# Kernel optimization log

Hardware: AMD Instinct MI355X
Metric: run time of the kernel (lower is better)

The kernel has to match this reference:

```python
import jax, jax.numpy as jnp
import numpy as np

B, N, D, P, H, DH = 1, 1536, 512, 64, 16, 64
INNER = H * DH  # 1024

def _ln(x, g, b, eps=1e-5):
    m = jnp.mean(x, axis=-1, keepdims=True)
    v = jnp.var(x, axis=-1, keepdims=True)
    return (x - m) / jnp.sqrt(v + eps) * g + b

def setup_inputs() -> dict:
    key = jax.random.key(0)
    ks = jax.random.split(key, 10)
    s = 0.02
    return {
        "node_feats": jax.random.normal(ks[0], (B, N, D), jnp.float32),
        "pair_feats": jax.random.normal(ks[1], (B, N, N, P), jnp.float32),
        "mask": jnp.ones((B, N, N), dtype=bool),
        "ln_node_g": jnp.ones((D,), jnp.float32), "ln_node_b": jnp.zeros((D,), jnp.float32),
        "ln_pair_g": jnp.ones((P,), jnp.float32), "ln_pair_b": jnp.zeros((P,), jnp.float32),
        "Wq": s * jax.random.normal(ks[2], (D, INNER), jnp.float32),
        "bq": jnp.zeros((INNER,), jnp.float32),
        "Wkv": s * jax.random.normal(ks[3], (D, 2 * INNER), jnp.float32),
        "bkv": jnp.zeros((2 * INNER,), jnp.float32),
        "qln_g": jnp.ones((INNER,), jnp.float32), "qln_b": jnp.zeros((INNER,), jnp.float32),
        "kln_g": jnp.ones((INNER,), jnp.float32), "kln_b": jnp.zeros((INNER,), jnp.float32),
        "Wg": s * jax.random.normal(ks[4], (D, INNER), jnp.float32),
        "bg": jnp.zeros((INNER,), jnp.float32),
        "Wbias": s * jax.random.normal(ks[5], (P, H), jnp.float32),
        "Wout": s * jax.random.normal(ks[6], (INNER, D), jnp.float32),
        "bout": jnp.zeros((D,), jnp.float32),
        "n_queries": 0,
        "n_keys": 0,
    }

def reference(node_feats, pair_feats, mask, ln_node_g, ln_node_b, ln_pair_g, ln_pair_b,
              Wq, bq, Wkv, bkv, qln_g, qln_b, kln_g, kln_b, Wg, bg, Wbias, Wout, bout,
              n_queries, n_keys):
    b, n, _ = node_feats.shape
    x = _ln(node_feats, ln_node_g, ln_node_b)          # [b,n,D]
    p = _ln(pair_feats, ln_pair_g, ln_pair_b)          # [b,n,n,P]
    q = _ln(x @ Wq + bq, qln_g, qln_b)                 # [b,n,I]
    kv = x @ Wkv + bkv
    k, v = jnp.split(kv, 2, axis=-1)
    k = _ln(k, kln_g, kln_b)
    g = x @ Wg + bg                                    # gating, [b,n,I]
    bias = jnp.einsum('bijp,ph->bhij', p, Wbias)       # pair bias, [b,h,n,n]
    # split heads -> [b,h,n,dh]
    split = lambda t: t.reshape(b, n, H, DH).transpose(0, 2, 1, 3)
    qh, kh, vh, gh = split(q), split(k), split(v), split(g)
    scale = DH ** -0.5
    sim = jnp.einsum('bhid,bhjd->bhij', qh, kh) * scale
    sim = jnp.where(mask[:, None, :, :], sim, jnp.finfo(sim.dtype).min)
    attn = jax.nn.softmax(sim + bias, axis=-1)
    o = jnp.einsum('bhij,bhjd->bhid', attn, vh)        # [b,h,n,dh]
    o = jax.nn.sigmoid(gh) * o
    o = o.transpose(0, 2, 1, 3).reshape(b, n, INNER)
    return o @ Wout + bout
```

## Files before the change

kernel.cpp:

```cpp
#include <hip/hip_runtime.h>

#define NN 1536
#define DD 512
#define PP 64
#define HH 16
#define DHD 64
#define INNER 1024
#define NCHUNK 4
#define JT_PER (NN / 64 / NCHUNK)

typedef __attribute__((ext_vector_type(4))) float f32x4;
typedef __attribute__((ext_vector_type(8))) _Float16 f16x8;
typedef __attribute__((ext_vector_type(4))) _Float16 f16x4;

__device__ inline float wave_sum(float v) {
#pragma unroll
  for (int m = 1; m <= 32; m <<= 1) v += __shfl_xor(v, m);
  return v;
}

__global__ __launch_bounds__(256) void transpose_f32_f16(const float* __restrict__ in,
    _Float16* __restrict__ out, int R, int C) {
  __shared__ float tile[64][65];
  int c0 = blockIdx.x * 64, r0 = blockIdx.y * 64;
  int tid = threadIdx.x;
  int ri = tid >> 4, ci = (tid & 15) * 4;
#pragma unroll
  for (int p = 0; p < 4; ++p) {
    float4 v = *(const float4*)&in[(size_t)(r0 + ri + p * 16) * C + c0 + ci];
    tile[ri + p * 16][ci + 0] = v.x;
    tile[ri + p * 16][ci + 1] = v.y;
    tile[ri + p * 16][ci + 2] = v.z;
    tile[ri + p * 16][ci + 3] = v.w;
  }
  __syncthreads();
  int wr = tid >> 3, wc = (tid & 7) * 8;
#pragma unroll
  for (int p = 0; p < 2; ++p) {
    f16x8 o;
#pragma unroll
    for (int jj = 0; jj < 8; ++jj) o[jj] = (_Float16)tile[wc + jj][wr + p * 32];
    *(f16x8*)&out[(size_t)(c0 + wr + p * 32) * R + r0 + wc] = o;
  }
}

__global__ __launch_bounds__(256) void transpose_qkvg(const float* __restrict__ Wq,
    const float* __restrict__ Wkv, const float* __restrict__ Wg,
    _Float16* __restrict__ BTall) {
  int cg0 = blockIdx.x * 64;
  const float* src; int Cs, c0;
  if (cg0 < 1024)      { src = Wq;  Cs = 1024; c0 = cg0; }
  else if (cg0 < 3072) { src = Wkv; Cs = 2048; c0 = cg0 - 1024; }
  else                 { src = Wg;  Cs = 1024; c0 = cg0 - 3072; }
  __shared__ float tile[64][65];
  int r0 = blockIdx.y * 64;
  int tid = threadIdx.x;
  int ri = tid >> 4, ci = (tid & 15) * 4;
#pragma unroll
  for (int p = 0; p < 4; ++p) {
    float4 v = *(const float4*)&src[(size_t)(r0 + ri + p * 16) * Cs + c0 + ci];
    tile[ri + p * 16][ci + 0] = v.x;
    tile[ri + p * 16][ci + 1] = v.y;
    tile[ri + p * 16][ci + 2] = v.z;
    tile[ri + p * 16][ci + 3] = v.w;
  }
  __syncthreads();
  int wr = tid >> 3, wc = (tid & 7) * 8;
#pragma unroll
  for (int p = 0; p < 2; ++p) {
    f16x8 o;
#pragma unroll
    for (int jj = 0; jj < 8; ++jj) o[jj] = (_Float16)tile[wc + jj][wr + p * 32];
    *(f16x8*)&BTall[(size_t)(cg0 + wr + p * 32) * DD + r0 + wc] = o;
  }
}

__global__ __launch_bounds__(256) void transpose_f16_b(const _Float16* __restrict__ in0,
    _Float16* __restrict__ out0, int R, int C) {
  const _Float16* in = in0 + (size_t)blockIdx.z * R * C;
  _Float16* out = out0 + (size_t)blockIdx.z * R * C;
  __shared__ _Float16 tile[64][72];
  int c0 = blockIdx.x * 64, r0 = blockIdx.y * 64;
  int tid = threadIdx.x;
  int ri = tid >> 3, ci = (tid & 7) * 8;
#pragma unroll
  for (int p = 0; p < 2; ++p)
    *(f16x8*)&tile[ri + p * 32][ci] = *(const f16x8*)&in[(size_t)(r0 + ri + p * 32) * C + c0 + ci];
  __syncthreads();
#pragma unroll
  for (int p = 0; p < 2; ++p) {
    f16x8 o;
#pragma unroll
    for (int jj = 0; jj < 8; ++jj) o[jj] = tile[ci + jj][ri + p * 32];
    *(f16x8*)&out[(size_t)(c0 + ri + p * 32) * R + r0 + ci] = o;
  }
}

__global__ __launch_bounds__(256) void node_ln_kernel(const float* __restrict__ nf,
    const float* __restrict__ g, const float* __restrict__ b, _Float16* __restrict__ x16) {
  int i = blockIdx.x, tid = threadIdx.x;
  int c = tid * 2;
  float2 v = *(const float2*)&nf[(size_t)i * DD + c];
  float s = v.x + v.y, ss = v.x * v.x + v.y * v.y;
  s = wave_sum(s); ss = wave_sum(ss);
  __shared__ float red[2][4];
  int w = tid >> 6;
  if ((tid & 63) == 0) { red[0][w] = s; red[1][w] = ss; }
  __syncthreads();
  s = red[0][0] + red[0][1] + red[0][2] + red[0][3];
  ss = red[1][0] + red[1][1] + red[1][2] + red[1][3];
  float mean = s * (1.f / DD);
  float var = ss * (1.f / DD) - mean * mean;
  float rstd = rsqrtf(var + 1e-5f);
  x16[(size_t)i * DD + c + 0] = (_Float16)((v.x - mean) * rstd * g[c + 0] + b[c + 0]);
  x16[(size_t)i * DD + c + 1] = (_Float16)((v.y - mean) * rstd * g[c + 1] + b[c + 1]);
}

__global__ __launch_bounds__(256) void gemm_proj(const _Float16* __restrict__ A,
    const _Float16* __restrict__ BT, const float* __restrict__ bq,
    const float* __restrict__ bkv, const float* __restrict__ bg,
    float* __restrict__ C) {
  __shared__ _Float16 As[64][72];
  __shared__ _Float16 Bs[64][72];
  int tid = threadIdx.x, lane = tid & 63, w = tid >> 6;
  int m0 = blockIdx.y * 64, n0 = blockIdx.x * 64;
  int wm = (w & 1) * 32, wn = (w >> 1) * 32;
  f32x4 acc[2][2] = {};
  int r = tid >> 3, c8 = (tid & 7) * 8;
  int lr = lane & 15, lg = lane >> 4;
  for (int k0 = 0; k0 < DD; k0 += 64) {
    *(f16x8*)&As[r][c8]      = *(const f16x8*)&A[(size_t)(m0 + r) * DD + k0 + c8];
    *(f16x8*)&As[r + 32][c8] = *(const f16x8*)&A[(size_t)(m0 + r + 32) * DD + k0 + c8];
    *(f16x8*)&Bs[r][c8]      = *(const f16x8*)&BT[(size_t)(n0 + r) * DD + k0 + c8];
    *(f16x8*)&Bs[r + 32][c8] = *(const f16x8*)&BT[(size_t)(n0 + r + 32) * DD + k0 + c8];
    __syncthreads();
#pragma unroll
    for (int kf = 0; kf < 2; ++kf) {
      f16x8 a0 = *(const f16x8*)&As[wm + lr][kf * 32 + lg * 8];
      f16x8 a1 = *(const f16x8*)&As[wm + 16 + lr][kf * 32 + lg * 8];
      f16x8 b0 = *(const f16x8*)&Bs[wn + lr][kf * 32 + lg * 8];
      f16x8 b1 = *(const f16x8*)&Bs[wn + 16 + lr][kf * 32 + lg * 8];
      acc[0][0] = __builtin_amdgcn_mfma_f32_16x16x32_f16(a0, b0, acc[0][0], 0, 0, 0);
      acc[0][1] = __builtin_amdgcn_mfma_f32_16x16x32_f16(a0, b1, acc[0][1], 0, 0, 0);
      acc[1][0] = __builtin_amdgcn_mfma_f32_16x16x32_f16(a1, b0, acc[1][0], 0, 0, 0);
      acc[1][1] = __builtin_amdgcn_mfma_f32_16x16x32_f16(a1, b1, acc[1][1], 0, 0, 0);
    }
    __syncthreads();
  }
#pragma unroll
  for (int mi = 0; mi < 2; ++mi)
#pragma unroll
    for (int ni = 0; ni < 2; ++ni)
#pragma unroll
      for (int rg = 0; rg < 4; ++rg) {
        int row = m0 + wm + mi * 16 + lg * 4 + rg;
        int col = n0 + wn + ni * 16 + lr;
        float bv = (col < 1024) ? bq[col] : (col < 3072) ? bkv[col - 1024] : bg[col - 3072];
        C[(size_t)row * 4096 + col] = acc[mi][ni][rg] + bv;
      }
}

__global__ __launch_bounds__(256) void gemm_f16(const _Float16* __restrict__ A,
    const _Float16* __restrict__ BT, const float* __restrict__ bias,
    float* __restrict__ C, int M, int N, int K) {
  __shared__ _Float16 As[64][72];
  __shared__ _Float16 Bs[64][72];
  int tid = threadIdx.x, lane = tid & 63, w = tid >> 6;
  int m0 = blockIdx.y * 64, n0 = blockIdx.x * 64;
  int wm = (w & 1) * 32, wn = (w >> 1) * 32;
  f32x4 acc[2][2] = {};
  int r = tid >> 3, c8 = (tid & 7) * 8;
  int lr = lane & 15, lg = lane >> 4;
  for (int k0 = 0; k0 < K; k0 += 64) {
    *(f16x8*)&As[r][c8]      = *(const f16x8*)&A[(size_t)(m0 + r) * K + k0 + c8];
    *(f16x8*)&As[r + 32][c8] = *(const f16x8*)&A[(size_t)(m0 + r + 32) * K + k0 + c8];
    *(f16x8*)&Bs[r][c8]      = *(const f16x8*)&BT[(size_t)(n0 + r) * K + k0 + c8];
    *(f16x8*)&Bs[r + 32][c8] = *(const f16x8*)&BT[(size_t)(n0 + r + 32) * K + k0 + c8];
    __syncthreads();
#pragma unroll
    for (int kf = 0; kf < 2; ++kf) {
      f16x8 a0 = *(const f16x8*)&As[wm + lr][kf * 32 + lg * 8];
      f16x8 a1 = *(const f16x8*)&As[wm + 16 + lr][kf * 32 + lg * 8];
      f16x8 b0 = *(const f16x8*)&Bs[wn + lr][kf * 32 + lg * 8];
      f16x8 b1 = *(const f16x8*)&Bs[wn + 16 + lr][kf * 32 + lg * 8];
      acc[0][0] = __builtin_amdgcn_mfma_f32_16x16x32_f16(a0, b0, acc[0][0], 0, 0, 0);
      acc[0][1] = __builtin_amdgcn_mfma_f32_16x16x32_f16(a0, b1, acc[0][1], 0, 0, 0);
      acc[1][0] = __builtin_amdgcn_mfma_f32_16x16x32_f16(a1, b0, acc[1][0], 0, 0, 0);
      acc[1][1] = __builtin_amdgcn_mfma_f32_16x16x32_f16(a1, b1, acc[1][1], 0, 0, 0);
    }
    __syncthreads();
  }
#pragma unroll
  for (int mi = 0; mi < 2; ++mi)
#pragma unroll
    for (int ni = 0; ni < 2; ++ni)
#pragma unroll
      for (int rg = 0; rg < 4; ++rg) {
        int row = m0 + wm + mi * 16 + lg * 4 + rg;
        int col = n0 + wn + ni * 16 + lr;
        C[(size_t)row * N + col] = acc[mi][ni][rg] + bias[col];
      }
}

__global__ __launch_bounds__(256) void qkv_ln_kernel(const float* __restrict__ prebuf,
    const float* __restrict__ qg, const float* __restrict__ qb,
    const float* __restrict__ kg, const float* __restrict__ kb,
    _Float16* __restrict__ q16, _Float16* __restrict__ k16, _Float16* __restrict__ v16) {
  int i = blockIdx.x, tid = threadIdx.x;
  int c = tid * 4;
  const float* rowp = &prebuf[(size_t)i * 4096];
  float4 qv = *(const float4*)&rowp[c];
  float4 kvv = *(const float4*)&rowp[1024 + c];
  float4 vv = *(const float4*)&rowp[2048 + c];
  float qs = qv.x + qv.y + qv.z + qv.w;
  float qss = qv.x * qv.x + qv.y * qv.y + qv.z * qv.z + qv.w * qv.w;
  float ks = kvv.x + kvv.y + kvv.z + kvv.w;
  float kss = kvv.x * kvv.x + kvv.y * kvv.y + kvv.z * kvv.z + kvv.w * kvv.w;
  qs = wave_sum(qs); qss = wave_sum(qss); ks = wave_sum(ks); kss = wave_sum(kss);
  __shared__ float red[4][4];
  int w = tid >> 6;
  if ((tid & 63) == 0) { red[0][w] = qs; red[1][w] = qss; red[2][w] = ks; red[3][w] = kss; }
  __syncthreads();
  qs = red[0][0] + red[0][1] + red[0][2] + red[0][3];
  qss = red[1][0] + red[1][1] + red[1][2] + red[1][3];
  ks = red[2][0] + red[2][1] + red[2][2] + red[2][3];
  kss = red[3][0] + red[3][1] + red[3][2] + red[3][3];
  float qm = qs * (1.f / INNER), qvr = qss * (1.f / INNER) - qm * qm, qr = rsqrtf(qvr + 1e-5f);
  float km = ks * (1.f / INNER), kvr = kss * (1.f / INNER) - km * km, kr = rsqrtf(kvr + 1e-5f);
  int hh = c >> 6, d = c & 63;
  size_t off = ((size_t)hh * NN + i) * DHD + d;
  f16x4 qo, ko, vo;
  qo[0] = (_Float16)((qv.x - qm) * qr * qg[c + 0] + qb[c + 0]);
  qo[1] = (_Float16)((qv.y - qm) * qr * qg[c + 1] + qb[c + 1]);
  qo[2] = (_Float16)((qv.z - qm) * qr * qg[c + 2] + qb[c + 2]);
  qo[3] = (_Float16)((qv.w - qm) * qr * qg[c + 3] + qb[c + 3]);
  ko[0] = (_Float16)((kvv.x - km) * kr * kg[c + 0] + kb[c + 0]);
  ko[1] = (_Float16)((kvv.y - km) * kr * kg[c + 1] + kb[c + 1]);
  ko[2] = (_Float16)((kvv.z - km) * kr * kg[c + 2] + kb[c + 2]);
  ko[3] = (_Float16)((kvv.w - km) * kr * kg[c + 3] + kb[c + 3]);
  vo[0] = (_Float16)vv.x; vo[1] = (_Float16)vv.y; vo[2] = (_Float16)vv.z; vo[3] = (_Float16)vv.w;
  *(f16x4*)&q16[off] = qo;
  *(f16x4*)&k16[off] = ko;
  *(f16x4*)&v16[off] = vo;
}

__global__ __launch_bounds__(256) void pair_bias_kernel(const float* __restrict__ pair,
    const float* __restrict__ pg, const float* __restrict__ pb,
    const float* __restrict__ Wbias, _Float16* __restrict__ bias16) {
  int i = blockIdx.x;
  int tid = threadIdx.x, lane = tid & 63, w = tid >> 6;
  int lj = lane & 15, pbase = (lane >> 4) * 8;
  f16x8 wb0, wb1;
#pragma unroll
  for (int jj = 0; jj < 8; ++jj) {
    wb0[jj] = (_Float16)Wbias[(pbase + jj) * HH + lj];
    wb1[jj] = (_Float16)Wbias[(pbase + 32 + jj) * HH + lj];
  }
  float4 g0 = *(const float4*)&pg[pbase],      g1 = *(const float4*)&pg[pbase + 4];
  float4 g2 = *(const float4*)&pg[pbase + 32], g3 = *(const float4*)&pg[pbase + 36];
  float4 b0 = *(const float4*)&pb[pbase],      b1 = *(const float4*)&pb[pbase + 4];
  float4 b2 = *(const float4*)&pb[pbase + 32], b3 = *(const float4*)&pb[pbase + 36];
  __shared__ _Float16 trans[16][72];
  for (int t4 = 0; t4 < 4; ++t4) {
    int jt0 = blockIdx.y * 256 + t4 * 64;
    int j = jt0 + w * 16 + lj;
    const float* src = &pair[((size_t)i * NN + j) * PP];
    float4 v0 = *(const float4*)&src[pbase];
    float4 v1 = *(const float4*)&src[pbase + 4];
    float4 v2 = *(const float4*)&src[pbase + 32];
    float4 v3 = *(const float4*)&src[pbase + 36];
    float s = v0.x + v0.y + v0.z + v0.w + v1.x + v1.y + v1.z + v1.w
            + v2.x + v2.y + v2.z + v2.w + v3.x + v3.y + v3.z + v3.w;
    float ss = v0.x * v0.x + v0.y * v0.y + v0.z * v0.z + v0.w * v0.w
             + v1.x * v1.x + v1.y * v1.y + v1.z * v1.z + v1.w * v1.w
             + v2.x * v2.x + v2.y * v2.y + v2.z * v2.z + v2.w * v2.w
             + v3.x * v3.x + v3.y * v3.y + v3.z * v3.z + v3.w * v3.w;
    s += __shfl_xor(s, 16); s += __shfl_xor(s, 32);
    ss += __shfl_xor(ss, 16); ss += __shfl_xor(ss, 32);
    float mean = s * (1.f / PP);
    float var = ss * (1.f / PP) - mean * mean;
    float rstd = rsqrtf(var + 1e-5f);
    f16x8 a0, a1;
    a0[0] = (_Float16)((v0.x - mean) * rstd * g0.x + b0.x);
    a0[1] = (_Float16)((v0.y - mean) * rstd * g0.y + b0.y);
    a0[2] = (_Float16)((v0.z - mean) * rstd * g0.z + b0.z);
    a0[3] = (_Float16)((v0.w - mean) * rstd * g0.w + b0.w);
    a0[4] = (_Float16)((v1.x - mean) * rstd * g1.x + b1.x);
    a0[5] = (_Float16)((v1.y - mean) * rstd * g1.y + b1.y);
    a0[6] = (_Float16)((v1.z - mean) * rstd * g1.z + b1.z);
    a0[7] = (_Float16)((v1.w - mean) * rstd * g1.w + b1.w);
    a1[0] = (_Float16)((v2.x - mean) * rstd * g2.x + b2.x);
    a1[1] = (_Float16)((v2.y - mean) * rstd * g2.y + b2.y);
    a1[2] = (_Float16)((v2.z - mean) * rstd * g2.z + b2.z);
    a1[3] = (_Float16)((v2.w - mean) * rstd * g2.w + b2.w);
    a1[4] = (_Float16)((v3.x - mean) * rstd * g3.x + b3.x);
    a1[5] = (_Float16)((v3.y - mean) * rstd * g3.y + b3.y);
    a1[6] = (_Float16)((v3.z - mean) * rstd * g3.z + b3.z);
    a1[7] = (_Float16)((v3.w - mean) * rstd * g3.w + b3.w);
    f32x4 cacc = {};
    cacc = __builtin_amdgcn_mfma_f32_16x16x32_f16(a0, wb0, cacc, 0, 0, 0);
    cacc = __builtin_amdgcn_mfma_f32_16x16x32_f16(a1, wb1, cacc, 0, 0, 0);
#pragma unroll
    for (int rg = 0; rg < 4; ++rg)
      trans[lj][w * 16 + (lane >> 4) * 4 + rg] = (_Float16)cacc[rg];
    __syncthreads();
    int hh = tid >> 4, jc = (tid & 15) * 4;
    f16x4 ov = *(const f16x4*)&trans[hh][jc];
    *(f16x4*)&bias16[((size_t)hh * NN + i) * NN + jt0 + jc] = ov;
    __syncthreads();
  }
}

__global__ __launch_bounds__(256) void attn_kernel(const _Float16* __restrict__ q16,
    const _Float16* __restrict__ k16, const _Float16* __restrict__ vT16,
    const _Float16* __restrict__ bias16, float* __restrict__ opart,
    float* __restrict__ mlbuf) {
  int it = blockIdx.x, h = blockIdx.y, ck = blockIdx.z;
  int tid = threadIdx.x, lane = tid & 63, w = tid >> 6;
  int lr = lane & 15, lg = lane >> 4;
  __shared__ _Float16 Kt[64][72];
  __shared__ _Float16 Vt[64][72];
  __shared__ _Float16 Bls[64][72];
  int ib0 = it * 64;
  int ib = ib0 + w * 16;
  f16x8 qb0 = *(const f16x8*)&q16[((size_t)h * NN + ib + lr) * DHD + lg * 8];
  f16x8 qb1 = *(const f16x8*)&q16[((size_t)h * NN + ib + lr) * DHD + 32 + lg * 8];
  float m = -INFINITY, lsum = 0.f;
  f32x4 oacc[4] = {};
  int sr = tid >> 3, sc = (tid & 7) * 8;
  for (int jt = ck * JT_PER; jt < (ck + 1) * JT_PER; ++jt) {
    int j0 = jt * 64;
    *(f16x8*)&Kt[sr][sc]      = *(const f16x8*)&k16[((size_t)h * NN + j0 + sr) * DHD + sc];
    *(f16x8*)&Kt[sr + 32][sc] = *(const f16x8*)&k16[((size_t)h * NN + j0 + sr + 32) * DHD + sc];
    *(f16x8*)&Vt[sr][sc]      = *(const f16x8*)&vT16[((size_t)h * DHD + sr) * NN + j0 + sc];
    *(f16x8*)&Vt[sr + 32][sc] = *(const f16x8*)&vT16[((size_t)h * DHD + sr + 32) * NN + j0 + sc];
    *(f16x8*)&Bls[sr][sc]      = *(const f16x8*)&bias16[((size_t)h * NN + ib0 + sr) * NN + j0 + sc];
    *(f16x8*)&Bls[sr + 32][sc] = *(const f16x8*)&bias16[((size_t)h * NN + ib0 + sr + 32) * NN + j0 + sc];
    __syncthreads();
    float s[4][4];
#pragma unroll
    for (int jq = 0; jq < 4; ++jq) {
      f16x8 ka0 = *(const f16x8*)&Kt[jq * 16 + lr][lg * 8];
      f16x8 ka1 = *(const f16x8*)&Kt[jq * 16 + lr][32 + lg * 8];
      f32x4 c = {};
      c = __builtin_amdgcn_mfma_f32_16x16x32_f16(ka0, qb0, c, 0, 0, 0);
      c = __builtin_amdgcn_mfma_f32_16x16x32_f16(ka1, qb1, c, 0, 0, 0);
      f16x4 bls = *(const f16x4*)&Bls[w * 16 + lr][jq * 16 + lg * 4];
#pragma unroll
      for (int r = 0; r < 4; ++r)
        s[jq][r] = c[r] * 0.125f + (float)bls[r];
    }
    float tmax = s[0][0];
#pragma unroll
    for (int jq = 0; jq < 4; ++jq)
#pragma unroll
      for (int r = 0; r < 4; ++r) tmax = fmaxf(tmax, s[jq][r]);
    tmax = fmaxf(tmax, __shfl_xor(tmax, 16));
    tmax = fmaxf(tmax, __shfl_xor(tmax, 32));
    float mn = fmaxf(m, tmax);
    float alpha = __expf(m - mn);
    float ps = 0.f;
    f16x4 pf[4];
#pragma unroll
    for (int jq = 0; jq < 4; ++jq)
#pragma unroll
      for (int r = 0; r < 4; ++r) {
        float p = __expf(s[jq][r] - mn);
        ps += p;
        pf[jq][r] = (_Float16)p;
      }
    ps += __shfl_xor(ps, 16);
    ps += __shfl_xor(ps, 32);
    lsum = lsum * alpha + ps;
    m = mn;
    float ar[4];
#pragma unroll
    for (int r = 0; r < 4; ++r) ar[r] = __shfl(alpha, lg * 4 + r);
#pragma unroll
    for (int dt = 0; dt < 4; ++dt)
#pragma unroll
      for (int r = 0; r < 4; ++r) oacc[dt][r] *= ar[r];
#pragma unroll
    for (int dt = 0; dt < 4; ++dt)
#pragma unroll
      for (int jq = 0; jq < 4; ++jq) {
        f16x4 vb = *(const f16x4*)&Vt[dt * 16 + lr][jq * 16 + lg * 4];
        oacc[dt] = __builtin_amdgcn_mfma_f32_16x16x16f16(pf[jq], vb, oacc[dt], 0, 0, 0);
      }
    __syncthreads();
  }
  size_t pbase = (((size_t)it * HH + h) * NCHUNK + ck) * 4096 + (size_t)w * 1024;
#pragma unroll
  for (int dt = 0; dt < 4; ++dt)
    *(f32x4*)&opart[pbase + dt * 256 + lane * 4] = oacc[dt];
  if (lg == 0) {
    size_t mb = (((size_t)it * HH + h) * NCHUNK + ck) * 128;
    mlbuf[mb + w * 16 + lr] = m;
    mlbuf[mb + 64 + w * 16 + lr] = lsum;
  }
}

__global__ __launch_bounds__(256) void attn_merge(const float* __restrict__ opart,
    const float* __restrict__ mlbuf, const float* __restrict__ prebuf,
    _Float16* __restrict__ o16) {
  int it = blockIdx.x, h = blockIdx.y;
  int tid = threadIdx.x, lane = tid & 63, w = tid >> 6;
  int lr = lane & 15, lg = lane >> 4;
  __shared__ float sm[NCHUNK][64], sl[NCHUNK][64];
  {
    int c = tid >> 6, i = tid & 63;
    size_t mb = (((size_t)it * HH + h) * NCHUNK + c) * 128;
    sm[c][i] = mlbuf[mb + i];
    sl[c][i] = mlbuf[mb + 64 + i];
  }
  __syncthreads();
  float wc[NCHUNK][4], linv[4];
#pragma unroll
  for (int r = 0; r < 4; ++r) {
    int i_loc = w * 16 + lg * 4 + r;
    float mg = sm[0][i_loc];
#pragma unroll
    for (int c = 1; c < NCHUNK; ++c) mg = fmaxf(mg, sm[c][i_loc]);
    float lt = 0.f;
#pragma unroll
    for (int c = 0; c < NCHUNK; ++c) {
      float e = __expf(sm[c][i_loc] - mg);
      wc[c][r] = e;
      lt += e * sl[c][i_loc];
    }
    linv[r] = 1.f / lt;
  }
  size_t base = ((size_t)it * HH + h) * NCHUNK * 4096 + (size_t)w * 1024;
#pragma unroll
  for (int dt = 0; dt < 4; ++dt) {
    f32x4 o = {};
#pragma unroll
    for (int c = 0; c < NCHUNK; ++c) {
      f32x4 v = *(const f32x4*)&opart[base + (size_t)c * 4096 + dt * 256 + lane * 4];
#pragma unroll
      for (int r = 0; r < 4; ++r) o[r] += wc[c][r] * v[r];
    }
    int d = dt * 16 + lr;
#pragma unroll
    for (int r = 0; r < 4; ++r) {
      int i = it * 64 + w * 16 + lg * 4 + r;
      float gt = prebuf[(size_t)i * 4096 + 3072 + h * DHD + d];
      float val = o[r] * linv[r] * (1.f / (1.f + __expf(-gt)));
      o16[(size_t)i * INNER + h * DHD + d] = (_Float16)val;
    }
  }
}

extern "C" void kernel_launch(void* const* d_in, const int* in_sizes, int n_in,
                              void* d_out, int out_size, void* d_ws, size_t ws_size,
                              hipStream_t stream) {
  const float* node  = (const float*)d_in[0];
  const float* pair  = (const float*)d_in[1];
  const float* ln_ng = (const float*)d_in[3];
  const float* ln_nb = (const float*)d_in[4];
  const float* ln_pg = (const float*)d_in[5];
  const float* ln_pb = (const float*)d_in[6];
  const float* Wq    = (const float*)d_in[7];
  const float* bq    = (const float*)d_in[8];
  const float* Wkv   = (const float*)d_in[9];
  const float* bkv   = (const float*)d_in[10];
  const float* qlg   = (const float*)d_in[11];
  const float* qlb   = (const float*)d_in[12];
  const float* klg   = (const float*)d_in[13];
  const float* klb   = (const float*)d_in[14];
  const float* Wg    = (const float*)d_in[15];
  const float* bg    = (const float*)d_in[16];
  const float* Wbias = (const float*)d_in[17];
  const float* Wout  = (const float*)d_in[18];
  const float* bout  = (const float*)d_in[19];
  float* out = (float*)d_out;

  char* ws = (char*)d_ws;
  const size_t MB = 1u << 20;
  _Float16* BTall  = (_Float16*)(ws + 0 * MB);
  _Float16* WoutT  = (_Float16*)(ws + 4 * MB);
  _Float16* x16    = (_Float16*)(ws + 5 * MB);
  float*    prebuf = (float*)(ws + 8 * MB);
  _Float16* q16    = (_Float16*)(ws + 32 * MB);
  _Float16* k16    = (_Float16*)(ws + 35 * MB);
  _Float16* v16    = (_Float16*)(ws + 38 * MB);
  _Float16* vT16   = (_Float16*)(ws + 41 * MB);
  _Float16* o16    = (_Float16*)(ws + 44 * MB);
  _Float16* bias16 = (_Float16*)(ws + 48 * MB);
  float*    opart  = (float*)(ws + 124 * MB);
  float*    mlbuf  = (float*)(ws + 150 * MB);

  transpose_qkvg<<<dim3(4096 / 64, DD / 64), 256, 0, stream>>>(Wq, Wkv, Wg, BTall);
  transpose_f32_f16<<<dim3(DD / 64, INNER / 64), 256, 0, stream>>>(Wout, WoutT, INNER, DD);

  node_ln_kernel<<<NN, 256, 0, stream>>>(node, ln_ng, ln_nb, x16);

  gemm_proj<<<dim3(4096 / 64, NN / 64), 256, 0, stream>>>(x16, BTall, bq, bkv, bg, prebuf);

  qkv_ln_kernel<<<NN, 256, 0, stream>>>(prebuf, qlg, qlb, klg, klb, q16, k16, v16);

  transpose_f16_b<<<dim3(1, NN / 64, HH), 256, 0, stream>>>(v16, vT16, NN, DHD);

  pair_bias_kernel<<<dim3(NN, NN / 256), 256, 0, stream>>>(pair, ln_pg, ln_pb, Wbias, bias16);

  attn_kernel<<<dim3(NN / 64, HH, NCHUNK), 256, 0, stream>>>(q16, k16, vT16, bias16, opart, mlbuf);

  attn_merge<<<dim3(NN / 64, HH), 256, 0, stream>>>(opart, mlbuf, prebuf, o16);

  gemm_f16<<<dim3(DD / 64, NN / 64), 256, 0, stream>>>(o16, WoutT, bout, out, NN, DD, INNER);
}
```

Measured before the change: 278.8 us.

## Fuse pair-bias LayerNorm projection into attention and store intermediates in fp16

Pair LayerNorm and the bias projection now run inside the attention kernel. Each block handles 16 query rows by 192 keys for all 16 heads and keeps the bias tile in LDS, so the 75MB fp16 bias tensor is never written to or read back from global memory. The projection buffer and the partial outputs are now stored in fp16, and the key range is split into 8 chunks instead of 4. K and V are read straight from global or L2 instead of being staged in LDS, and the larger register footprint may lower occupancy.

```diff
diff --git a/kernel.cpp b/kernel.cpp
--- a/kernel.cpp
+++ b/kernel.cpp
@@ -6,8 +6,12 @@
 #define HH 16
 #define DHD 64
 #define INNER 1024
-#define NCHUNK 4
-#define JT_PER (NN / 64 / NCHUNK)
+#define NJ 8
+#define JT_PER 3
+#define ITILE 16
+#define NIT (NN / ITILE)
+#define BIS 68
+#define BHS 1092
 
 typedef __attribute__((ext_vector_type(4))) float f32x4;
 typedef __attribute__((ext_vector_type(8))) _Float16 f16x8;
@@ -119,7 +123,7 @@
 __global__ __launch_bounds__(256) void gemm_proj(const _Float16* __restrict__ A,
     const _Float16* __restrict__ BT, const float* __restrict__ bq,
     const float* __restrict__ bkv, const float* __restrict__ bg,
-    float* __restrict__ C) {
+    _Float16* __restrict__ C) {
   __shared__ _Float16 As[64][72];
   __shared__ _Float16 Bs[64][72];
   int tid = threadIdx.x, lane = tid & 63, w = tid >> 6;
@@ -156,7 +160,7 @@
         int row = m0 + wm + mi * 16 + lg * 4 + rg;
         int col = n0 + wn + ni * 16 + lr;
         float bv = (col < 1024) ? bq[col] : (col < 3072) ? bkv[col - 1024] : bg[col - 3072];
-        C[(size_t)row * 4096 + col] = acc[mi][ni][rg] + bv;
+        C[(size_t)row * 4096 + col] = (_Float16)(acc[mi][ni][rg] + bv);
       }
 }
 
@@ -202,20 +206,23 @@
       }
 }
 
-__global__ __launch_bounds__(256) void qkv_ln_kernel(const float* __restrict__ prebuf,
+__global__ __launch_bounds__(256) void qkv_ln_kernel(const _Float16* __restrict__ prebuf,
     const float* __restrict__ qg, const float* __restrict__ qb,
     const float* __restrict__ kg, const float* __restrict__ kb,
     _Float16* __restrict__ q16, _Float16* __restrict__ k16, _Float16* __restrict__ v16) {
   int i = blockIdx.x, tid = threadIdx.x;
   int c = tid * 4;
-  const float* rowp = &prebuf[(size_t)i * 4096];
-  float4 qv = *(const float4*)&rowp[c];
-  float4 kvv = *(const float4*)&rowp[1024 + c];
-  float4 vv = *(const float4*)&rowp[2048 + c];
-  float qs = qv.x + qv.y + qv.z + qv.w;
-  float qss = qv.x * qv.x + qv.y * qv.y + qv.z * qv.z + qv.w * qv.w;
-  float ks = kvv.x + kvv.y + kvv.z + kvv.w;
-  float kss = kvv.x * kvv.x + kvv.y * kvv.y + kvv.z * kvv.z + kvv.w * kvv.w;
+  const _Float16* rowp = &prebuf[(size_t)i * 4096];
+  f16x4 qh = *(const f16x4*)&rowp[c];
+  f16x4 kh = *(const f16x4*)&rowp[1024 + c];
+  f16x4 vh = *(const f16x4*)&rowp[2048 + c];
+  float qv[4], kv[4];
+#pragma unroll
+  for (int e = 0; e < 4; ++e) { qv[e] = (float)qh[e]; kv[e] = (float)kh[e]; }
+  float qs = qv[0] + qv[1] + qv[2] + qv[3];
+  float qss = qv[0] * qv[0] + qv[1] * qv[1] + qv[2] * qv[2] + qv[3] * qv[3];
+  float ks = kv[0] + kv[1] + kv[2] + kv[3];
+  float kss = kv[0] * kv[0] + kv[1] * kv[1] + kv[2] * kv[2] + kv[3] * kv[3];
   qs = wave_sum(qs); qss = wave_sum(qss); ks = wave_sum(ks); kss = wave_sum(kss);
   __shared__ float red[4][4];
   int w = tid >> 6;
@@ -229,225 +236,210 @@
   float km = ks * (1.f / INNER), kvr = kss * (1.f / INNER) - km * km, kr = rsqrtf(kvr + 1e-5f);
   int hh = c >> 6, d = c & 63;
   size_t off = ((size_t)hh * NN + i) * DHD + d;
-  f16x4 qo, ko, vo;
-  qo[0] = (_Float16)((qv.x - qm) * qr * qg[c + 0] + qb[c + 0]);
-  qo[1] = (_Float16)((qv.y - qm) * qr * qg[c + 1] + qb[c + 1]);
-  qo[2] = (_Float16)((qv.z - qm) * qr * qg[c + 2] + qb[c + 2]);
-  qo[3] = (_Float16)((qv.w - qm) * qr * qg[c + 3] + qb[c + 3]);
-  ko[0] = (_Float16)((kvv.x - km) * kr * kg[c + 0] + kb[c + 0]);
-  ko[1] = (_Float16)((kvv.y - km) * kr * kg[c + 1] + kb[c + 1]);
-  ko[2] = (_Float16)((kvv.z - km) * kr * kg[c + 2] + kb[c + 2]);
-  ko[3] = (_Float16)((kvv.w - km) * kr * kg[c + 3] + kb[c + 3]);
-  vo[0] = (_Float16)vv.x; vo[1] = (_Float16)vv.y; vo[2] = (_Float16)vv.z; vo[3] = (_Float16)vv.w;
+  f16x4 qo, ko;
+#pragma unroll
+  for (int e = 0; e < 4; ++e) {
+    qo[e] = (_Float16)((qv[e] - qm) * qr * qg[c + e] + qb[c + e]);
+    ko[e] = (_Float16)((kv[e] - km) * kr * kg[c + e] + kb[c + e]);
+  }
   *(f16x4*)&q16[off] = qo;
   *(f16x4*)&k16[off] = ko;
-  *(f16x4*)&v16[off] = vo;
-}
-
-__global__ __launch_bounds__(256) void pair_bias_kernel(const float* __restrict__ pair,
+  *(f16x4*)&v16[off] = vh;
+}
+
+__global__ __launch_bounds__(256, 2) void fused_pair_attn(const float* __restrict__ pair,
     const float* __restrict__ pg, const float* __restrict__ pb,
-    const float* __restrict__ Wbias, _Float16* __restrict__ bias16) {
-  int i = blockIdx.x;
-  int tid = threadIdx.x, lane = tid & 63, w = tid >> 6;
-  int lj = lane & 15, pbase = (lane >> 4) * 8;
-  f16x8 wb0, wb1;
-#pragma unroll
-  for (int jj = 0; jj < 8; ++jj) {
-    wb0[jj] = (_Float16)Wbias[(pbase + jj) * HH + lj];
-    wb1[jj] = (_Float16)Wbias[(pbase + 32 + jj) * HH + lj];
-  }
-  float4 g0 = *(const float4*)&pg[pbase],      g1 = *(const float4*)&pg[pbase + 4];
-  float4 g2 = *(const float4*)&pg[pbase + 32], g3 = *(const float4*)&pg[pbase + 36];
-  float4 b0 = *(const float4*)&pb[pbase],      b1 = *(const float4*)&pb[pbase + 4];
-  float4 b2 = *(const float4*)&pb[pbase + 32], b3 = *(const float4*)&pb[pbase + 36];
-  __shared__ _Float16 trans[16][72];
-  for (int t4 = 0; t4 < 4; ++t4) {
-    int jt0 = blockIdx.y * 256 + t4 * 64;
-    int j = jt0 + w * 16 + lj;
-    const float* src = &pair[((size_t)i * NN + j) * PP];
-    float4 v0 = *(const float4*)&src[pbase];
-    float4 v1 = *(const float4*)&src[pbase + 4];
-    float4 v2 = *(const float4*)&src[pbase + 32];
-    float4 v3 = *(const float4*)&src[pbase + 36];
-    float s = v0.x + v0.y + v0.z + v0.w + v1.x + v1.y + v1.z + v1.w
-            + v2.x + v2.y + v2.z + v2.w + v3.x + v3.y + v3.z + v3.w;
-    float ss = v0.x * v0.x + v0.y * v0.y + v0.z * v0.z + v0.w * v0.w
-             + v1.x * v1.x + v1.y * v1.y + v1.z * v1.z + v1.w * v1.w
-             + v2.x * v2.x + v2.y * v2.y + v2.z * v2.z + v2.w * v2.w
-             + v3.x * v3.x + v3.y * v3.y + v3.z * v3.z + v3.w * v3.w;
-    s += __shfl_xor(s, 16); s += __shfl_xor(s, 32);
-    ss += __shfl_xor(ss, 16); ss += __shfl_xor(ss, 32);
-    float mean = s * (1.f / PP);
-    float var = ss * (1.f / PP) - mean * mean;
-    float rstd = rsqrtf(var + 1e-5f);
-    f16x8 a0, a1;
-    a0[0] = (_Float16)((v0.x - mean) * rstd * g0.x + b0.x);
-    a0[1] = (_Float16)((v0.y - mean) * rstd * g0.y + b0.y);
-    a0[2] = (_Float16)((v0.z - mean) * rstd * g0.z + b0.z);
-    a0[3] = (_Float16)((v0.w - mean) * rstd * g0.w + b0.w);
-    a0[4] = (_Float16)((v1.x - mean) * rstd * g1.x + b1.x);
-    a0[5] = (_Float16)((v1.y - mean) * rstd * g1.y + b1.y);
-    a0[6] = (_Float16)((v1.z - mean) * rstd * g1.z + b1.z);
-    a0[7] = (_Float16)((v1.w - mean) * rstd * g1.w + b1.w);
-    a1[0] = (_Float16)((v2.x - mean) * rstd * g2.x + b2.x);
-    a1[1] = (_Float16)((v2.y - mean) * rstd * g2.y + b2.y);
-    a1[2] = (_Float16)((v2.z - mean) * rstd * g2.z + b2.z);
-    a1[3] = (_Float16)((v2.w - mean) * rstd * g2.w + b2.w);
-    a1[4] = (_Float16)((v3.x - mean) * rstd * g3.x + b3.x);
-    a1[5] = (_Float16)((v3.y - mean) * rstd * g3.y + b3.y);
-    a1[6] = (_Float16)((v3.z - mean) * rstd * g3.z + b3.z);
-    a1[7] = (_Float16)((v3.w - mean) * rstd * g3.w + b3.w);
-    f32x4 cacc = {};
-    cacc = __builtin_amdgcn_mfma_f32_16x16x32_f16(a0, wb0, cacc, 0, 0, 0);
-    cacc = __builtin_amdgcn_mfma_f32_16x16x32_f16(a1, wb1, cacc, 0, 0, 0);
-#pragma unroll
-    for (int rg = 0; rg < 4; ++rg)
-      trans[lj][w * 16 + (lane >> 4) * 4 + rg] = (_Float16)cacc[rg];
-    __syncthreads();
-    int hh = tid >> 4, jc = (tid & 15) * 4;
-    f16x4 ov = *(const f16x4*)&trans[hh][jc];
-    *(f16x4*)&bias16[((size_t)hh * NN + i) * NN + jt0 + jc] = ov;
-    __syncthreads();
-  }
-}
-
-__global__ __launch_bounds__(256) void attn_kernel(const _Float16* __restrict__ q16,
+    const float* __restrict__ Wbias, const _Float16* __restrict__ q16,
     const _Float16* __restrict__ k16, const _Float16* __restrict__ vT16,
-    const _Float16* __restrict__ bias16, float* __restrict__ opart,
-    float* __restrict__ mlbuf) {
-  int it = blockIdx.x, h = blockIdx.y, ck = blockIdx.z;
+    _Float16* __restrict__ opart, float* __restrict__ mlbuf) {
+  int it = blockIdx.x, ck = blockIdx.y;
   int tid = threadIdx.x, lane = tid & 63, w = tid >> 6;
   int lr = lane & 15, lg = lane >> 4;
-  __shared__ _Float16 Kt[64][72];
-  __shared__ _Float16 Vt[64][72];
-  __shared__ _Float16 Bls[64][72];
-  int ib0 = it * 64;
-  int ib = ib0 + w * 16;
-  f16x8 qb0 = *(const f16x8*)&q16[((size_t)h * NN + ib + lr) * DHD + lg * 8];
-  f16x8 qb1 = *(const f16x8*)&q16[((size_t)h * NN + ib + lr) * DHD + 32 + lg * 8];
-  float m = -INFINITY, lsum = 0.f;
-  f32x4 oacc[4] = {};
-  int sr = tid >> 3, sc = (tid & 7) * 8;
-  for (int jt = ck * JT_PER; jt < (ck + 1) * JT_PER; ++jt) {
-    int j0 = jt * 64;
-    *(f16x8*)&Kt[sr][sc]      = *(const f16x8*)&k16[((size_t)h * NN + j0 + sr) * DHD + sc];
-    *(f16x8*)&Kt[sr + 32][sc] = *(const f16x8*)&k16[((size_t)h * NN + j0 + sr + 32) * DHD + sc];
-    *(f16x8*)&Vt[sr][sc]      = *(const f16x8*)&vT16[((size_t)h * DHD + sr) * NN + j0 + sc];
-    *(f16x8*)&Vt[sr + 32][sc] = *(const f16x8*)&vT16[((size_t)h * DHD + sr + 32) * NN + j0 + sc];
-    *(f16x8*)&Bls[sr][sc]      = *(const f16x8*)&bias16[((size_t)h * NN + ib0 + sr) * NN + j0 + sc];
-    *(f16x8*)&Bls[sr + 32][sc] = *(const f16x8*)&bias16[((size_t)h * NN + ib0 + sr + 32) * NN + j0 + sc];
-    __syncthreads();
-    float s[4][4];
-#pragma unroll
-    for (int jq = 0; jq < 4; ++jq) {
-      f16x8 ka0 = *(const f16x8*)&Kt[jq * 16 + lr][lg * 8];
-      f16x8 ka1 = *(const f16x8*)&Kt[jq * 16 + lr][32 + lg * 8];
-      f32x4 c = {};
-      c = __builtin_amdgcn_mfma_f32_16x16x32_f16(ka0, qb0, c, 0, 0, 0);
-      c = __builtin_amdgcn_mfma_f32_16x16x32_f16(ka1, qb1, c, 0, 0, 0);
-      f16x4 bls = *(const f16x4*)&Bls[w * 16 + lr][jq * 16 + lg * 4];
-#pragma unroll
-      for (int r = 0; r < 4; ++r)
-        s[jq][r] = c[r] * 0.125f + (float)bls[r];
-    }
-    float tmax = s[0][0];
-#pragma unroll
-    for (int jq = 0; jq < 4; ++jq)
-#pragma unroll
-      for (int r = 0; r < 4; ++r) tmax = fmaxf(tmax, s[jq][r]);
-    tmax = fmaxf(tmax, __shfl_xor(tmax, 16));
-    tmax = fmaxf(tmax, __shfl_xor(tmax, 32));
-    float mn = fmaxf(m, tmax);
-    float alpha = __expf(m - mn);
-    float ps = 0.f;
-    f16x4 pf[4];
-#pragma unroll
-    for (int jq = 0; jq < 4; ++jq)
-#pragma unroll
-      for (int r = 0; r < 4; ++r) {
-        float p = __expf(s[jq][r] - mn);
-        ps += p;
-        pf[jq][r] = (_Float16)p;
+  int ib0 = it * ITILE;
+  __shared__ _Float16 bias_lds[HH * BHS];
+
+  f16x8 wb0, wb1;
+#pragma unroll
+  for (int e = 0; e < 8; ++e) {
+    wb0[e] = (_Float16)Wbias[(lg * 8 + e) * HH + lr];
+    wb1[e] = (_Float16)Wbias[(32 + lg * 8 + e) * HH + lr];
+  }
+  float4 g0 = *(const float4*)&pg[lg * 8],      g1 = *(const float4*)&pg[lg * 8 + 4];
+  float4 g2 = *(const float4*)&pg[32 + lg * 8], g3 = *(const float4*)&pg[36 + lg * 8];
+  float4 b0 = *(const float4*)&pb[lg * 8],      b1 = *(const float4*)&pb[lg * 8 + 4];
+  float4 b2 = *(const float4*)&pb[32 + lg * 8], b3 = *(const float4*)&pb[36 + lg * 8];
+
+  float m[4], l[4];
+  f32x4 oacc[4][4] = {};
+#pragma unroll
+  for (int hh = 0; hh < 4; ++hh) { m[hh] = -INFINITY; l[hh] = 0.f; }
+
+  for (int jj = 0; jj < JT_PER; ++jj) {
+    int j0 = (ck * JT_PER + jj) * 64;
+    __syncthreads();
+    for (int t = 0; t < 16; ++t) {
+      const float* src = &pair[((size_t)(ib0 + t) * NN + (j0 + w * 16 + lr)) * PP];
+      float4 v0 = *(const float4*)&src[lg * 8];
+      float4 v1 = *(const float4*)&src[lg * 8 + 4];
+      float4 v2 = *(const float4*)&src[32 + lg * 8];
+      float4 v3 = *(const float4*)&src[36 + lg * 8];
+      float s = v0.x + v0.y + v0.z + v0.w + v1.x + v1.y + v1.z + v1.w
+              + v2.x + v2.y + v2.z + v2.w + v3.x + v3.y + v3.z + v3.w;
+      float ss = v0.x * v0.x + v0.y * v0.y + v0.z * v0.z + v0.w * v0.w
+               + v1.x * v1.x + v1.y * v1.y + v1.z * v1.z + v1.w * v1.w
+               + v2.x * v2.x + v2.y * v2.y + v2.z * v2.z + v2.w * v2.w
+               + v3.x * v3.x + v3.y * v3.y + v3.z * v3.z + v3.w * v3.w;
+      s += __shfl_xor(s, 16); s += __shfl_xor(s, 32);
+      ss += __shfl_xor(ss, 16); ss += __shfl_xor(ss, 32);
+      float mean = s * (1.f / PP);
+      float var = ss * (1.f / PP) - mean * mean;
+      float rstd = rsqrtf(var + 1e-5f);
+      f16x8 a0, a1;
+      a0[0] = (_Float16)((v0.x - mean) * rstd * g0.x + b0.x);
+      a0[1] = (_Float16)((v0.y - mean) * rstd * g0.y + b0.y);
+      a0[2] = (_Float16)((v0.z - mean) * rstd * g0.z + b0.z);
+      a0[3] = (_Float16)((v0.w - mean) * rstd * g0.w + b0.w);
+      a0[4] = (_Float16)((v1.x - mean) * rstd * g1.x + b1.x);
+      a0[5] = (_Float16)((v1.y - mean) * rstd * g1.y + b1.y);
+      a0[6] = (_Float16)((v1.z - mean) * rstd * g1.z + b1.z);
+      a0[7] = (_Float16)((v1.w - mean) * rstd * g1.w + b1.w);
+      a1[0] = (_Float16)((v2.x - mean) * rstd * g2.x + b2.x);
+      a1[1] = (_Float16)((v2.y - mean) * rstd * g2.y + b2.y);
+      a1[2] = (_Float16)((v2.z - mean) * rstd * g2.z + b2.z);
+      a1[3] = (_Float16)((v2.w - mean) * rstd * g2.w + b2.w);
+      a1[4] = (_Float16)((v3.x - mean) * rstd * g3.x + b3.x);
+      a1[5] = (_Float16)((v3.y - mean) * rstd * g3.y + b3.y);
+      a1[6] = (_Float16)((v3.z - mean) * rstd * g3.z + b3.z);
+      a1[7] = (_Float16)((v3.w - mean) * rstd * g3.w + b3.w);
+      f32x4 cacc = {};
+      cacc = __builtin_amdgcn_mfma_f32_16x16x32_f16(a0, wb0, cacc, 0, 0, 0);
+      cacc = __builtin_amdgcn_mfma_f32_16x16x32_f16(a1, wb1, cacc, 0, 0, 0);
+      f16x4 bv;
+#pragma unroll
+      for (int r = 0; r < 4; ++r) bv[r] = (_Float16)cacc[r];
+      *(f16x4*)&bias_lds[lr * BHS + t * BIS + w * 16 + lg * 4] = bv;
+    }
+    __syncthreads();
+#pragma unroll
+    for (int hh = 0; hh < 4; ++hh) {
+      int h = w * 4 + hh;
+      f16x8 qb0 = *(const f16x8*)&q16[((size_t)h * NN + ib0 + lr) * DHD + lg * 8];
+      f16x8 qb1 = *(const f16x8*)&q16[((size_t)h * NN + ib0 + lr) * DHD + 32 + lg * 8];
+      float s[4][4];
+#pragma unroll
+      for (int jq = 0; jq < 4; ++jq) {
+        f16x8 ka0 = *(const f16x8*)&k16[((size_t)h * NN + j0 + jq * 16 + lr) * DHD + lg * 8];
+        f16x8 ka1 = *(const f16x8*)&k16[((size_t)h * NN + j0 + jq * 16 + lr) * DHD + 32 + lg * 8];
+        f32x4 c = {};
+        c = __builtin_amdgcn_mfma_f32_16x16x32_f16(ka0, qb0, c, 0, 0, 0);
+        c = __builtin_amdgcn_mfma_f32_16x16x32_f16(ka1, qb1, c, 0, 0, 0);
+        f16x4 bls = *(const f16x4*)&bias_lds[h * BHS + lr * BIS + jq * 16 + lg * 4];
+#pragma unroll
+        for (int r = 0; r < 4; ++r)
+          s[jq][r] = c[r] * 0.125f + (float)bls[r];
       }
-    ps += __shfl_xor(ps, 16);
-    ps += __shfl_xor(ps, 32);
-    lsum = lsum * alpha + ps;
-    m = mn;
-    float ar[4];
-#pragma unroll
-    for (int r = 0; r < 4; ++r) ar[r] = __shfl(alpha, lg * 4 + r);
-#pragma unroll
-    for (int dt = 0; dt < 4; ++dt)
-#pragma unroll
-      for (int r = 0; r < 4; ++r) oacc[dt][r] *= ar[r];
-#pragma unroll
-    for (int dt = 0; dt < 4; ++dt)
-#pragma unroll
-      for (int jq = 0; jq < 4; ++jq) {
-        f16x4 vb = *(const f16x4*)&Vt[dt * 16 + lr][jq * 16 + lg * 4];
-        oacc[dt] = __builtin_amdgcn_mfma_f32_16x16x16f16(pf[jq], vb, oacc[dt], 0, 0, 0);
-      }
-    __syncthreads();
-  }
-  size_t pbase = (((size_t)it * HH + h) * NCHUNK + ck) * 4096 + (size_t)w * 1024;
-#pragma unroll
-  for (int dt = 0; dt < 4; ++dt)
-    *(f32x4*)&opart[pbase + dt * 256 + lane * 4] = oacc[dt];
-  if (lg == 0) {
-    size_t mb = (((size_t)it * HH + h) * NCHUNK + ck) * 128;
-    mlbuf[mb + w * 16 + lr] = m;
-    mlbuf[mb + 64 + w * 16 + lr] = lsum;
-  }
-}
-
-__global__ __launch_bounds__(256) void attn_merge(const float* __restrict__ opart,
-    const float* __restrict__ mlbuf, const float* __restrict__ prebuf,
+      float tmax = s[0][0];
+#pragma unroll
+      for (int jq = 0; jq < 4; ++jq)
+#pragma unroll
+        for (int r = 0; r < 4; ++r) tmax = fmaxf(tmax, s[jq][r]);
+      tmax = fmaxf(tmax, __shfl_xor(tmax, 16));
+      tmax = fmaxf(tmax, __shfl_xor(tmax, 32));
+      float mn = fmaxf(m[hh], tmax);
+      float alpha = __expf(m[hh] - mn);
+      float ps = 0.f;
+      f16x4 pf[4];
+#pragma unroll
+      for (int jq = 0; jq < 4; ++jq)
+#pragma unroll
+        for (int r = 0; r < 4; ++r) {
+          float p = __expf(s[jq][r] - mn);
+          ps += p;
+          pf[jq][r] = (_Float16)p;
+        }
+      ps += __shfl_xor(ps, 16);
+      ps += __shfl_xor(ps, 32);
+      l[hh] = l[hh] * alpha + ps;
+      m[hh] = mn;
+      float ar[4];
+#pragma unroll
+      for (int r = 0; r < 4; ++r) ar[r] = __shfl(alpha, lg * 4 + r);
+#pragma unroll
+      for (int dt = 0; dt < 4; ++dt)
+#pragma unroll
+        for (int r = 0; r < 4; ++r) oacc[hh][dt][r] *= ar[r];
+#pragma unroll
+      for (int dt = 0; dt < 4; ++dt)
+#pragma unroll
+        for (int jq = 0; jq < 4; ++jq) {
+          f16x4 vb = *(const f16x4*)&vT16[((size_t)h * DHD + dt * 16 + lr) * NN + j0 + jq * 16 + lg * 4];
+          oacc[hh][dt] = __builtin_amdgcn_mfma_f32_16x16x16f16(pf[jq], vb, oacc[hh][dt], 0, 0, 0);
+        }
+    }
+  }
+#pragma unroll
+  for (int hh = 0; hh < 4; ++hh) {
+    int h = w * 4 + hh;
+    size_t base = (((size_t)it * HH + h) * NJ + ck) * 1024;
+#pragma unroll
+    for (int dt = 0; dt < 4; ++dt) {
+      f16x4 ov;
+#pragma unroll
+      for (int r = 0; r < 4; ++r) ov[r] = (_Float16)oacc[hh][dt][r];
+      *(f16x4*)&opart[base + (dt * 16 + lr) * 16 + lg * 4] = ov;
+    }
+    if (lg == 0) {
+      size_t mb = (((size_t)it * HH + h) * NJ + ck) * 32;
+      mlbuf[mb + lr] = m[hh];
+      mlbuf[mb + 16 + lr] = l[hh];
+    }
+  }
+}
+
+__global__ __launch_bounds__(256) void attn_merge(const _Float16* __restrict__ opart,
+    const float* __restrict__ mlbuf, const _Float16* __restrict__ prebuf,
     _Float16* __restrict__ o16) {
   int it = blockIdx.x, h = blockIdx.y;
-  int tid = threadIdx.x, lane = tid & 63, w = tid >> 6;
-  int lr = lane & 15, lg = lane >> 4;
-  __shared__ float sm[NCHUNK][64], sl[NCHUNK][64];
+  int tid = threadIdx.x;
+  __shared__ float sm[NJ][16], sl[NJ][16];
   {
-    int c = tid >> 6, i = tid & 63;
-    size_t mb = (((size_t)it * HH + h) * NCHUNK + c) * 128;
-    sm[c][i] = mlbuf[mb + i];
-    sl[c][i] = mlbuf[mb + 64 + i];
-  }
-  __syncthreads();
-  float wc[NCHUNK][4], linv[4];
+    int ck = tid >> 5, r = tid & 31;
+    size_t mb = (((size_t)it * HH + h) * NJ + ck) * 32;
+    if (r < 16) sm[ck][r] = mlbuf[mb + r];
+    else        sl[ck][r - 16] = mlbuf[mb + r];
+  }
+  __syncthreads();
+  int d = tid >> 2, ig = (tid & 3) * 4;
+  float wc[NJ][4], linv[4];
 #pragma unroll
   for (int r = 0; r < 4; ++r) {
-    int i_loc = w * 16 + lg * 4 + r;
-    float mg = sm[0][i_loc];
-#pragma unroll
-    for (int c = 1; c < NCHUNK; ++c) mg = fmaxf(mg, sm[c][i_loc]);
+    int i = ig + r;
+    float mg = sm[0][i];
+#pragma unroll
+    for (int c = 1; c < NJ; ++c) mg = fmaxf(mg, sm[c][i]);
     float lt = 0.f;
 #pragma unroll
-    for (int c = 0; c < NCHUNK; ++c) {
-      float e = __expf(sm[c][i_loc] - mg);
+    for (int c = 0; c < NJ; ++c) {
+      float e = __expf(sm[c][i] - mg);
       wc[c][r] = e;
-      lt += e * sl[c][i_loc];
+      lt += e * sl[c][i];
     }
     linv[r] = 1.f / lt;
   }
-  size_t base = ((size_t)it * HH + h) * NCHUNK * 4096 + (size_t)w * 1024;
-#pragma unroll
-  for (int dt = 0; dt < 4; ++dt) {
-    f32x4 o = {};
-#pragma unroll
-    for (int c = 0; c < NCHUNK; ++c) {
-      f32x4 v = *(const f32x4*)&opart[base + (size_t)c * 4096 + dt * 256 + lane * 4];
-#pragma unroll
-      for (int r = 0; r < 4; ++r) o[r] += wc[c][r] * v[r];
-    }
-    int d = dt * 16 + lr;
-#pragma unroll
-    for (int r = 0; r < 4; ++r) {
-      int i = it * 64 + w * 16 + lg * 4 + r;
-      float gt = prebuf[(size_t)i * 4096 + 3072 + h * DHD + d];
-      float val = o[r] * linv[r] * (1.f / (1.f + __expf(-gt)));
-      o16[(size_t)i * INNER + h * DHD + d] = (_Float16)val;
-    }
+  size_t base = ((size_t)it * HH + h) * NJ * 1024;
+  float o[4] = {};
+#pragma unroll
+  for (int c = 0; c < NJ; ++c) {
+    f16x4 v = *(const f16x4*)&opart[base + (size_t)c * 1024 + d * 16 + ig];
+#pragma unroll
+    for (int r = 0; r < 4; ++r) o[r] += wc[c][r] * (float)v[r];
+  }
+#pragma unroll
+  for (int r = 0; r < 4; ++r) {
+    int i = it * ITILE + ig + r;
+    float gt = (float)prebuf[(size_t)i * 4096 + 3072 + h * DHD + d];
+    float val = o[r] * linv[r] * (1.f / (1.f + __expf(-gt)));
+    o16[(size_t)i * INNER + h * DHD + d] = (_Float16)val;
   }
 }
 
@@ -477,35 +469,28 @@
 
   char* ws = (char*)d_ws;
   const size_t MB = 1u << 20;
-  _Float16* BTall  = (_Float16*)(ws + 0 * MB);
-  _Float16* WoutT  = (_Float16*)(ws + 4 * MB);
-  _Float16* x16    = (_Float16*)(ws + 5 * MB);
-  float*    prebuf = (float*)(ws + 8 * MB);
-  _Float16* q16    = (_Float16*)(ws + 32 * MB);
-  _Float16* k16    = (_Float16*)(ws + 35 * MB);
-  _Float16* v16    = (_Float16*)(ws + 38 * MB);
-  _Float16* vT16   = (_Float16*)(ws + 41 * MB);
-  _Float16* o16    = (_Float16*)(ws + 44 * MB);
-  _Float16* bias16 = (_Float16*)(ws + 48 * MB);
-  float*    opart  = (float*)(ws + 124 * MB);
-  float*    mlbuf  = (float*)(ws + 150 * MB);
+  _Float16* BTall    = (_Float16*)(ws + 0 * MB);
+  _Float16* WoutT    = (_Float16*)(ws + 4 * MB);
+  _Float16* x16      = (_Float16*)(ws + 5 * MB);
+  _Float16* prebuf16 = (_Float16*)(ws + 8 * MB);
+  _Float16* q16      = (_Float16*)(ws + 20 * MB);
+  _Float16* k16      = (_Float16*)(ws + 23 * MB);
+  _Float16* v16      = (_Float16*)(ws + 26 * MB);
+  _Float16* vT16     = (_Float16*)(ws + 29 * MB);
+  _Float16* o16      = (_Float16*)(ws + 32 * MB);
+  _Float16* opart    = (_Float16*)(ws + 36 * MB);
+  float*    mlbuf    = (float*)(ws + 62 * MB);
 
   transpose_qkvg<<<dim3(4096 / 64, DD / 64), 256, 0, stream>>>(Wq, Wkv, Wg, BTall);
   transpose_f32_f16<<<dim3(DD / 64, INNER / 64), 256, 0, stream>>>(Wout, WoutT, INNER, DD);
-
   node_ln_kernel<<<NN, 256, 0, stream>>>(node, ln_ng, ln_nb, x16);
-
-  gemm_proj<<<dim3(4096 / 64, NN / 64), 256, 0, stream>>>(x16, BTall, bq, bkv, bg, prebuf);
-
-  qkv_ln_kernel<<<NN, 256, 0, stream>>>(prebuf, qlg, qlb, klg, klb, q16, k16, v16);
-
+  gemm_proj<<<dim3(4096 / 64, NN / 64), 256, 0, stream>>>(x16, BTall, bq, bkv, bg, prebuf16);
+  qkv_ln_kernel<<<NN, 256, 0, stream>>>(prebuf16, qlg, qlb, klg, klb, q16, k16, v16);
   transpose_f16_b<<<dim3(1, NN / 64, HH), 256, 0, stream>>>(v16, vT16, NN, DHD);
 
-  pair_bias_kernel<<<dim3(NN, NN / 256), 256, 0, stream>>>(pair, ln_pg, ln_pb, Wbias, bias16);
-
-  attn_kernel<<<dim3(NN / 64, HH, NCHUNK), 256, 0, stream>>>(q16, k16, vT16, bias16, opart, mlbuf);
-
-  attn_merge<<<dim3(NN / 64, HH), 256, 0, stream>>>(opart, mlbuf, prebuf, o16);
+  fused_pair_attn<<<dim3(NIT, NJ), 256, 0, stream>>>(pair, ln_pg, ln_pb, Wbias,
+                                                     q16, k16, vT16, opart, mlbuf);
+  attn_merge<<<dim3(NIT, HH), 256, 0, stream>>>(opart, mlbuf, prebuf16, o16);
 
   gemm_f16<<<dim3(DD / 64, NN / 64), 256, 0, stream>>>(o16, WoutT, bout, out, NN, DD, INNER);
 }
```

Result: slower. 340.8 us (+22.2%).
